# Kernel optimization log

Measured on AMD Instinct MI355X. Metric: run time of the kernel, lower is better.

The kernel has to match this reference:

```python
import jax, jax.numpy as jnp
import numpy as np

B, T, E, H = 4, 4096, 1024, 64  # batch, seq_len, embed dim, head_size


def setup_inputs() -> dict:
    key = jax.random.key(0)
    kx, kk, kq, kv = jax.random.split(key, 4)
    x = jax.random.normal(kx, (B, T, E), dtype=jnp.float32)
    # nn.Linear(E, H, bias=False) weight, stored here as [E, H] (x @ W)
    Wk = jax.random.normal(kk, (E, H), dtype=jnp.float32) * 0.02
    Wq = jax.random.normal(kq, (E, H), dtype=jnp.float32) * 0.02
    Wv = jax.random.normal(kv, (E, H), dtype=jnp.float32) * 0.02
    return {"x": x, "Wk": Wk, "Wq": Wq, "Wv": Wv}


def reference(x, Wk, Wq, Wv):
    # single-head scaled dot-product attention (dropout p=0 -> identity)
    k = jnp.einsum("bte,eh->bth", x, Wk)
    q = jnp.einsum("bte,eh->bth", x, Wq)
    v = jnp.einsum("bte,eh->bth", x, Wv)
    scale = jnp.asarray(H, x.dtype) ** -0.5
    wei = jnp.einsum("bqh,bkh->bqk", q, k) * scale  # [B,T,T]
    wei = jax.nn.softmax(wei, axis=-1)
    out = jnp.einsum("bqk,bkh->bqh", wei, v)  # [B,T,H]
    return out
```

## Files before the change

### kernel.cpp

```cpp
#include <hip/hip_runtime.h>
#include <hip/hip_bf16.h>


typedef __attribute__((ext_vector_type(8))) short short8;
typedef __attribute__((ext_vector_type(4))) short short4v;
typedef __attribute__((ext_vector_type(4))) float f32x4;
typedef __attribute__((ext_vector_type(2))) unsigned uint2v;

#define LOG2E 1.44269504f

__device__ inline short f2bf(float f) {
  union { __hip_bfloat16 h; short s; } u; u.h = __float2bfloat16(f); return u.s;
}
__device__ inline unsigned cvt_pk_bf16(float lo, float hi) {
  unsigned r;
  asm("v_cvt_pk_bf16_f32 %0, %1, %2" : "=v"(r) : "v"(lo), "v"(hi));
  return r;
}
__device__ inline void gl_lds16(const short* g, short* l) {
  __builtin_amdgcn_global_load_lds(
      (const __attribute__((address_space(1))) void*)g,
      (__attribute__((address_space(3))) void*)l, 16, 0, 0);
}
__device__ inline float xsum4g(float x) {
  uint2v a = __builtin_amdgcn_permlane32_swap(__float_as_uint(x), __float_as_uint(x), false, false);
  float y = __uint_as_float(a[0]) + __uint_as_float(a[1]);
  uint2v b = __builtin_amdgcn_permlane16_swap(__float_as_uint(y), __float_as_uint(y), false, false);
  return __uint_as_float(b[0]) + __uint_as_float(b[1]);
}

__global__ __launch_bounds__(256) void wtrans_kernel(
    const float* __restrict__ Wk, const float* __restrict__ Wq, const float* __restrict__ Wv,
    short* __restrict__ wT)
{
  const int m3 = blockIdx.y;
  const float* W = (m3 == 0) ? Wk : (m3 == 1) ? Wq : Wv;
  const float sc = (m3 == 1) ? 0.125f * LOG2E : 1.0f;
  int idx = blockIdx.x * 256 + threadIdx.x;
  int k = idx >> 6;
  int n = idx & 63;
  wT[(size_t)m3 * 65536 + n * 1024 + k] = f2bf(W[idx] * sc);
}

__global__ __launch_bounds__(256) void proj_kernel(
    const float* __restrict__ x, const short* __restrict__ wT,
    short* __restrict__ kout, short* __restrict__ qout, short* __restrict__ vTout)
{
  const int m3 = blockIdx.y;
  __shared__ __align__(16) short xl[64][72];
  __shared__ __align__(16) short wl[64][64];

  const int tid  = threadIdx.x;
  const int w    = tid >> 6;
  const int lane = tid & 63;
  const int lr   = lane & 15;
  const int lg   = lane >> 4;
  const int rowbase = blockIdx.x * 64;
  const short* wb = wT + (size_t)m3 * 65536;

  f32x4 acc[4];
#pragma unroll
  for (int j = 0; j < 4; ++j) acc[j] = (f32x4){0.f, 0.f, 0.f, 0.f};

  const int xr = tid >> 4;
  const int xc = (tid & 15) << 2;

  float4 nx[4];
  short8 nw[2];
#pragma unroll
  for (int p = 0; p < 4; ++p)
    nx[p] = *reinterpret_cast<const float4*>(&x[(size_t)(rowbase + xr + p * 16) * 1024 + xc]);
#pragma unroll
  for (int p = 0; p < 2; ++p) {
    int c = p * 256 + tid;
    nw[p] = *reinterpret_cast<const short8*>(&wb[(size_t)(c >> 3) * 1024 + ((c & 7) << 3)]);
  }

  for (int t = 0; t < 16; ++t) {
    if (t > 0) __syncthreads();

#pragma unroll
    for (int p = 0; p < 4; ++p) {
      uint2v pk;
      pk[0] = cvt_pk_bf16(nx[p].x, nx[p].y);
      pk[1] = cvt_pk_bf16(nx[p].z, nx[p].w);
      *reinterpret_cast<uint2v*>(&xl[xr + p * 16][xc]) = pk;
    }
#pragma unroll
    for (int p = 0; p < 2; ++p) {
      int c = p * 256 + tid;
      int n = c >> 3;
      int kk = (c & 7) << 3;
      *reinterpret_cast<short8*>(&wl[n][kk ^ ((n & 7) << 3)]) = nw[p];
    }
    __syncthreads();

    if (t < 15) {
      const int kb = (t + 1) * 64;
#pragma unroll
      for (int p = 0; p < 4; ++p)
        nx[p] = *reinterpret_cast<const float4*>(
            &x[(size_t)(rowbase + xr + p * 16) * 1024 + kb + xc]);
#pragma unroll
      for (int p = 0; p < 2; ++p) {
        int c = p * 256 + tid;
        nw[p] = *reinterpret_cast<const short8*>(
            &wb[(size_t)(c >> 3) * 1024 + kb + ((c & 7) << 3)]);
      }
    }

#pragma unroll
    for (int ks = 0; ks < 2; ++ks) {
      short8 a = *reinterpret_cast<const short8*>(&xl[16 * w + lr][ks * 32 + lg * 8]);
#pragma unroll
      for (int ct = 0; ct < 4; ++ct) {
        short8 b = *reinterpret_cast<const short8*>(
            &wl[16 * ct + lr][(ks * 32 + lg * 8) ^ ((lr & 7) << 3)]);
        acc[ct] = __builtin_amdgcn_mfma_f32_16x16x32_bf16(a, b, acc[ct], 0, 0, 0);
      }
    }
  }

  if (m3 == 2) {
    const int bb   = rowbase >> 12;
    const int tloc = (rowbase & 4095) + 16 * w + 4 * lg;
#pragma unroll
    for (int ct = 0; ct < 4; ++ct) {
      uint2v pk;
      pk[0] = cvt_pk_bf16(acc[ct][0], acc[ct][1]);
      pk[1] = cvt_pk_bf16(acc[ct][2], acc[ct][3]);
      size_t vidx = (size_t)bb * 64 * 4096 + (size_t)(16 * ct + lr) * 4096 + tloc;
      *reinterpret_cast<uint2v*>(&vTout[vidx]) = pk;
    }
  } else {
    short* out = (m3 == 0) ? kout : qout;
#pragma unroll
    for (int ct = 0; ct < 4; ++ct)
#pragma unroll
      for (int j = 0; j < 4; ++j) {
        int grow = rowbase + 16 * w + 4 * lg + j;
        out[(size_t)grow * 64 + 16 * ct + lr] = f2bf(acc[ct][j]);
      }
  }
}

__device__ __forceinline__ void softmax_t(f32x4 s[4], float& l, short8 pf[2]) {
#pragma unroll
  for (int a = 0; a < 4; ++a)
#pragma unroll
    for (int j = 0; j < 4; ++j) s[a][j] = __builtin_amdgcn_exp2f(s[a][j]);
  float ps = ((s[0][0] + s[0][1]) + (s[0][2] + s[0][3]))
           + ((s[1][0] + s[1][1]) + (s[1][2] + s[1][3]))
           + ((s[2][0] + s[2][1]) + (s[2][2] + s[2][3]))
           + ((s[3][0] + s[3][1]) + (s[3][2] + s[3][3]));
  l += ps;

  unsigned u[4][2];
#pragma unroll
  for (int a = 0; a < 4; ++a) {
    u[a][0] = cvt_pk_bf16(s[a][0], s[a][1]);
    u[a][1] = cvt_pk_bf16(s[a][2], s[a][3]);
  }
  unsigned t[2][4];
#pragma unroll
  for (int k1 = 0; k1 < 2; ++k1)
#pragma unroll
    for (int jj = 0; jj < 2; ++jj) {
      uint2v A = __builtin_amdgcn_permlane32_swap(u[2 * k1][jj], u[2 * k1 + 1][jj], false, false);
      uint2v T = __builtin_amdgcn_permlane16_swap(A[0], A[1], false, false);
      t[k1][jj]     = T[0];
      t[k1][2 + jj] = T[1];
    }
#pragma unroll
  for (int ks = 0; ks < 2; ++ks) {
    union { unsigned u4[4]; short8 s8; } cv;
    cv.u4[0] = t[ks][0]; cv.u4[1] = t[ks][1]; cv.u4[2] = t[ks][2]; cv.u4[3] = t[ks][3];
    pf[ks] = cv.s8;
  }
}

__global__ __launch_bounds__(512, 4) void attn_split_kernel(
    const short* __restrict__ qm, const short* __restrict__ km, const short* __restrict__ vT,
    float* __restrict__ opart, float* __restrict__ lpart,
    int S, int chunkTiles)
{
  int qidx, split;
  if (S == 8) {
    const int xcd = (int)blockIdx.x & 7;
    const int idx = (int)blockIdx.x >> 3;
    split = (xcd & 1) * 4 + (idx & 3);
    qidx  = (xcd >> 1) * 16 + (idx >> 2);
  } else {
    const int nwg = 64 * S;
    int bid = (int)blockIdx.x;
    bid = (bid & 7) * (nwg >> 3) + (bid >> 3);
    qidx = bid / S; split = bid % S;
  }
  const int b  = qidx >> 4;
  const int qt = qidx & 15;
  const int tid  = threadIdx.x;
  const int w    = tid >> 6;
  const int lane = tid & 63;
  const int lr   = lane & 15;
  const int lg   = lane >> 4;

  __shared__ __align__(16) short kl[2][4096];
  __shared__ __align__(16) short vl[2][4096];

  const short* qb    = qm + ((size_t)(b * 4096 + qt * 256 + w * 32)) * 64;
  const short* kbase = km + (size_t)b * 262144;
  const short* vbase = vT + (size_t)b * 262144;

  const int lrow = lane >> 3;
  const int scol = ((lane & 7) * 8) ^ (lrow * 8);
  const int swr  = (lr & 7) << 3;

  auto stage = [&](int buf, int kt) {
    const short* kp = kbase + (size_t)kt * 4096;
    gl_lds16(kp + (8 * w + lrow) * 64 + scol, &kl[buf][w * 512]);
    const short* vp = vbase + (size_t)kt * 64;
    gl_lds16(vp + (size_t)(8 * w + lrow) * 4096 + scol, &vl[buf][w * 512]);
  };

  short8 qf0[2], qf1[2];
#pragma unroll
  for (int ks = 0; ks < 2; ++ks) {
    qf0[ks] = *reinterpret_cast<const short8*>(&qb[lr * 64 + ks * 32 + lg * 8]);
    qf1[ks] = *reinterpret_cast<const short8*>(&qb[(16 + lr) * 64 + ks * 32 + lg * 8]);
  }

  float l0 = 0.f, l1 = 0.f;
  f32x4 o0[4], o1[4];
#pragma unroll
  for (int dt = 0; dt < 4; ++dt) {
    o0[dt] = (f32x4){0.f, 0.f, 0.f, 0.f};
    o1[dt] = (f32x4){0.f, 0.f, 0.f, 0.f};
  }

  const int kt0 = split * chunkTiles;
  stage(0, kt0);
  __syncthreads();

  for (int it = 0; it < chunkTiles; ++it) {
    const int  cur  = it & 1;
    const bool more = (it + 1) < chunkTiles;
    if (more) stage(cur ^ 1, kt0 + it + 1);

    const short* klc = kl[cur];
    const short* vlc = vl[cur];

    f32x4 s0[4], s1[4];
#pragma unroll
    for (int a = 0; a < 4; ++a) {
      s0[a] = (f32x4){0.f, 0.f, 0.f, 0.f};
      s1[a] = (f32x4){0.f, 0.f, 0.f, 0.f};
    }
    __builtin_amdgcn_s_setprio(1);
#pragma unroll
    for (int ks = 0; ks < 2; ++ks)
#pragma unroll
      for (int kt16 = 0; kt16 < 4; ++kt16) {
        short8 kf = *reinterpret_cast<const short8*>(
            &klc[(kt16 * 16 + lr) * 64 + ((ks * 32 + lg * 8) ^ swr)]);
        s0[kt16] = __builtin_amdgcn_mfma_f32_16x16x32_bf16(kf, qf0[ks], s0[kt16], 0, 0, 0);
        s1[kt16] = __builtin_amdgcn_mfma_f32_16x16x32_bf16(kf, qf1[ks], s1[kt16], 0, 0, 0);
      }
    __builtin_amdgcn_s_setprio(0);

    short8 pf0[2], pf1[2];
    softmax_t(s0, l0, pf0);
    softmax_t(s1, l1, pf1);

    __builtin_amdgcn_s_setprio(1);
#pragma unroll
    for (int ks = 0; ks < 2; ++ks)
#pragma unroll
      for (int dt = 0; dt < 4; ++dt) {
        short8 vf = *reinterpret_cast<const short8*>(
            &vlc[(dt * 16 + lr) * 64 + ((ks * 32 + lg * 8) ^ swr)]);
        o0[dt] = __builtin_amdgcn_mfma_f32_16x16x32_bf16(vf, pf0[ks], o0[dt], 0, 0, 0);
        o1[dt] = __builtin_amdgcn_mfma_f32_16x16x32_bf16(vf, pf1[ks], o1[dt], 0, 0, 0);
      }
    __builtin_amdgcn_s_setprio(0);

    if (more) __syncthreads();
  }

  l0 = xsum4g(l0);
  l1 = xsum4g(l1);
  const int rowg = b * 4096 + qt * 256 + w * 32 + lr;
  float* ob0 = opart + ((size_t)split * 16384 + rowg) * 64;
  float* ob1 = ob0 + 16 * 64;
#pragma unroll
  for (int dt = 0; dt < 4; ++dt) {
    *reinterpret_cast<f32x4*>(&ob0[16 * dt + 4 * lg]) = o0[dt];
    *reinterpret_cast<f32x4*>(&ob1[16 * dt + 4 * lg]) = o1[dt];
  }
  if (lane < 16) {
    lpart[split * 16384 + rowg]      = l0;
    lpart[split * 16384 + rowg + 16] = l1;
  }
}

__global__ __launch_bounds__(256) void merge_kernel(
    const float* __restrict__ opart, const float* __restrict__ lpart,
    float* __restrict__ out, int S)
{
  int gid = blockIdx.x * 256 + threadIdx.x;
  int row = gid >> 4;
  int c4  = (gid & 15) << 2;
  float denom = 0.f;
  float ax = 0.f, ay = 0.f, az = 0.f, aw = 0.f;
  for (int s = 0; s < S; ++s) {
    denom += lpart[s * 16384 + row];
    float4 op = *reinterpret_cast<const float4*>(&opart[((size_t)s * 16384 + row) * 64 + c4]);
    ax += op.x; ay += op.y; az += op.z; aw += op.w;
  }
  float inv = 1.f / denom;
  float4 r; r.x = ax * inv; r.y = ay * inv; r.z = az * inv; r.w = aw * inv;
  *reinterpret_cast<float4*>(&out[(size_t)row * 64 + c4]) = r;
}

extern "C" void kernel_launch(void* const* d_in, const int* in_sizes, int n_in,
                              void* d_out, int out_size, void* d_ws, size_t ws_size,
                              hipStream_t stream) {
  const float* x  = (const float*)d_in[0];
  const float* Wk = (const float*)d_in[1];
  const float* Wq = (const float*)d_in[2];
  const float* Wv = (const float*)d_in[3];

  const size_t MH = (size_t)16384 * 64;
  short* kmat = (short*)d_ws;
  short* qmat = kmat + MH;
  short* vTm  = qmat + MH;
  short* wT   = vTm + MH;

  dim3 gw(256, 3);
  wtrans_kernel<<<gw, 256, 0, stream>>>(Wk, Wq, Wv, wT);
  dim3 gproj(256, 3);
  proj_kernel<<<gproj, 256, 0, stream>>>(x, wT, kmat, qmat, vTm);

  const size_t head_bytes = (3 * MH + 196608) * sizeof(short);
  const size_t o_bytes    = MH * sizeof(float);
  const size_t l_bytes    = (size_t)16384 * sizeof(float);
  int S = 8;
  while (S > 1 && head_bytes + (size_t)S * (o_bytes + l_bytes) > ws_size) S >>= 1;

  float* opart = (float*)((char*)d_ws + head_bytes);
  float* lpart = opart + (size_t)S * MH;
  attn_split_kernel<<<64 * S, 512, 0, stream>>>(qmat, kmat, vTm,
                                                opart, lpart, S, 64 / S);
  merge_kernel<<<1024, 256, 0, stream>>>(opart, lpart, (float*)d_out, S);
}
```

Before: 56.83 us.

## Load x fragments directly into MFMA registers and double-buffer weight tiles in LDS

The projection kernel now has each lane load its own x fragment straight from global memory and convert it to bf16 in registers, so x no longer goes through LDS. Weight tiles are double-buffered in LDS, which cuts the loop to one barrier per k-step instead of two. This removes the LDS write/read traffic for x and one sync per iteration. In exchange, the x global loads are less coalesced: each lane reads 32-byte pieces from a different row.

```diff
diff --git a/kernel.cpp b/kernel.cpp
--- a/kernel.cpp
+++ b/kernel.cpp
@@ -47,8 +47,7 @@
     short* __restrict__ kout, short* __restrict__ qout, short* __restrict__ vTout)
 {
   const int m3 = blockIdx.y;
-  __shared__ __align__(16) short xl[64][72];
-  __shared__ __align__(16) short wl[64][64];
+  __shared__ __align__(16) short wl[2][4096];
 
   const int tid  = threadIdx.x;
   const int w    = tid >> 6;
@@ -58,66 +57,69 @@
   const int rowbase = blockIdx.x * 64;
   const short* wb = wT + (size_t)m3 * 65536;
 
+  const int n0  = tid >> 3;
+  const int kk0 = (tid & 7) << 3;
+
+  const float* xrow = x + (size_t)(rowbase + 16 * w + lr) * 1024;
+
   f32x4 acc[4];
 #pragma unroll
   for (int j = 0; j < 4; ++j) acc[j] = (f32x4){0.f, 0.f, 0.f, 0.f};
 
-  const int xr = tid >> 4;
-  const int xc = (tid & 15) << 2;
-
-  float4 nx[4];
+  f32x4 xf[2][2], nxf[2][2];
   short8 nw[2];
 #pragma unroll
-  for (int p = 0; p < 4; ++p)
-    nx[p] = *reinterpret_cast<const float4*>(&x[(size_t)(rowbase + xr + p * 16) * 1024 + xc]);
-#pragma unroll
-  for (int p = 0; p < 2; ++p) {
-    int c = p * 256 + tid;
-    nw[p] = *reinterpret_cast<const short8*>(&wb[(size_t)(c >> 3) * 1024 + ((c & 7) << 3)]);
-  }
+  for (int ks = 0; ks < 2; ++ks)
+#pragma unroll
+    for (int i = 0; i < 2; ++i)
+      xf[ks][i] = *reinterpret_cast<const f32x4*>(xrow + ks * 32 + lg * 8 + i * 4);
+  nw[0] = *reinterpret_cast<const short8*>(&wb[(size_t)n0 * 1024 + kk0]);
+  nw[1] = *reinterpret_cast<const short8*>(&wb[(size_t)(n0 + 32) * 1024 + kk0]);
+  *reinterpret_cast<short8*>(&wl[0][n0 * 64 + (kk0 ^ ((n0 & 7) << 3))])          = nw[0];
+  *reinterpret_cast<short8*>(&wl[0][(n0 + 32) * 64 + (kk0 ^ ((n0 & 7) << 3))])   = nw[1];
+  __syncthreads();
 
   for (int t = 0; t < 16; ++t) {
-    if (t > 0) __syncthreads();
-
-#pragma unroll
-    for (int p = 0; p < 4; ++p) {
-      uint2v pk;
-      pk[0] = cvt_pk_bf16(nx[p].x, nx[p].y);
-      pk[1] = cvt_pk_bf16(nx[p].z, nx[p].w);
-      *reinterpret_cast<uint2v*>(&xl[xr + p * 16][xc]) = pk;
-    }
-#pragma unroll
-    for (int p = 0; p < 2; ++p) {
-      int c = p * 256 + tid;
-      int n = c >> 3;
-      int kk = (c & 7) << 3;
-      *reinterpret_cast<short8*>(&wl[n][kk ^ ((n & 7) << 3)]) = nw[p];
-    }
-    __syncthreads();
-
-    if (t < 15) {
+    const int cur = t & 1;
+    const bool more = (t + 1) < 16;
+
+    if (more) {
       const int kb = (t + 1) * 64;
 #pragma unroll
-      for (int p = 0; p < 4; ++p)
-        nx[p] = *reinterpret_cast<const float4*>(
-            &x[(size_t)(rowbase + xr + p * 16) * 1024 + kb + xc]);
-#pragma unroll
-      for (int p = 0; p < 2; ++p) {
-        int c = p * 256 + tid;
-        nw[p] = *reinterpret_cast<const short8*>(
-            &wb[(size_t)(c >> 3) * 1024 + kb + ((c & 7) << 3)]);
-      }
+      for (int ks = 0; ks < 2; ++ks)
+#pragma unroll
+        for (int i = 0; i < 2; ++i)
+          nxf[ks][i] = *reinterpret_cast<const f32x4*>(xrow + kb + ks * 32 + lg * 8 + i * 4);
+      nw[0] = *reinterpret_cast<const short8*>(&wb[(size_t)n0 * 1024 + kb + kk0]);
+      nw[1] = *reinterpret_cast<const short8*>(&wb[(size_t)(n0 + 32) * 1024 + kb + kk0]);
     }
 
 #pragma unroll
     for (int ks = 0; ks < 2; ++ks) {
-      short8 a = *reinterpret_cast<const short8*>(&xl[16 * w + lr][ks * 32 + lg * 8]);
+      union { unsigned u4[4]; short8 s8; } cva;
+      cva.u4[0] = cvt_pk_bf16(xf[ks][0][0], xf[ks][0][1]);
+      cva.u4[1] = cvt_pk_bf16(xf[ks][0][2], xf[ks][0][3]);
+      cva.u4[2] = cvt_pk_bf16(xf[ks][1][0], xf[ks][1][1]);
+      cva.u4[3] = cvt_pk_bf16(xf[ks][1][2], xf[ks][1][3]);
+      short8 a = cva.s8;
 #pragma unroll
       for (int ct = 0; ct < 4; ++ct) {
         short8 b = *reinterpret_cast<const short8*>(
-            &wl[16 * ct + lr][(ks * 32 + lg * 8) ^ ((lr & 7) << 3)]);
+            &wl[cur][(16 * ct + lr) * 64 + ((ks * 32 + lg * 8) ^ ((lr & 7) << 3))]);
         acc[ct] = __builtin_amdgcn_mfma_f32_16x16x32_bf16(a, b, acc[ct], 0, 0, 0);
       }
+    }
+
+    if (more) {
+#pragma unroll
+      for (int ks = 0; ks < 2; ++ks)
+#pragma unroll
+        for (int i = 0; i < 2; ++i)
+          xf[ks][i] = nxf[ks][i];
+      const int nxt = cur ^ 1;
+      *reinterpret_cast<short8*>(&wl[nxt][n0 * 64 + (kk0 ^ ((n0 & 7) << 3))])        = nw[0];
+      *reinterpret_cast<short8*>(&wl[nxt][(n0 + 32) * 64 + (kk0 ^ ((n0 & 7) << 3))]) = nw[1];
+      __syncthreads();
     }
   }
 
```

After: 67.20 us. +18.2%, slower.
